# Kernel tuning notes

Hardware: AMD Instinct MI355X
Metric: run time of the kernel (lower is better)

The kernel has to match this reference:

```python
import jax, jax.numpy as jnp
import numpy as np

B, T, I, H = 512, 256, 256, 512

def setup_inputs() -> dict:
    key = jax.random.key(0)
    k1, k2, k3, k4, k5 = jax.random.split(key, 5)
    s = 1.0 / np.sqrt(H + I)
    return {
        "x": jax.random.normal(k1, (B, T, I), dtype=jnp.float32),
        "W_w": jax.random.normal(k2, (4 * H, H + I), dtype=jnp.float32) * s,
        "W_b": jax.random.normal(k3, (4 * H,), dtype=jnp.float32) * s,
        "fc_w": jax.random.normal(k4, (1, H), dtype=jnp.float32) * (1.0 / np.sqrt(H)),
        "fc_b": jax.random.normal(k5, (1,), dtype=jnp.float32) * 0.02,
    }

def reference(x, W_w, W_b, fc_w, fc_b):
    # combined = cat(h_prev, x_t): first H columns of W_w act on h, last I on x
    Wh = W_w[:, :H]          # [4H, H]
    Wx = W_w[:, H:]          # [4H, I]
    # precompute input contributions for all timesteps: [B, T, 4H]
    xW = jnp.einsum('bti,gi->btg', x, Wx) + W_b

    def step(carry, xw_t):
        h, c = carry
        gates = xw_t + h @ Wh.T                      # [B, 4H]
        f, i, o, c_hat = jnp.split(gates, 4, axis=1)  # chunk order f,i,o,c_hat
        f = jax.nn.sigmoid(f)
        i = jax.nn.sigmoid(i)
        o = jax.nn.sigmoid(o)
        c_hat = jnp.tanh(c_hat)
        c_new = f * c + i * c_hat
        h_new = o * jnp.tanh(c_new)
        return (h_new, c_new), None

    h0 = jnp.zeros((x.shape[0], H), dtype=x.dtype)
    c0 = jnp.zeros((x.shape[0], H), dtype=x.dtype)
    (h_T, _), _ = jax.lax.scan(step, (h0, c0), jnp.swapaxes(xW, 0, 1))
    return h_T @ fc_w.T + fc_b                       # [B, 1]
```

## Files before the change

kernel.cpp:

```cpp
#include <hip/hip_runtime.h>
#include <hip/hip_bf16.h>
#include <stdint.h>


#define B_SZ 512
#define T_SZ 256
#define I_SZ 256
#define H_SZ 512
#define K_SZ 768
#define BH   (B_SZ * H_SZ)

typedef float  f32x4  __attribute__((ext_vector_type(4)));
typedef __bf16 bf16x8 __attribute__((ext_vector_type(8)));

__device__ __forceinline__ float fast_sigmoid(float v) {
  return __builtin_amdgcn_rcpf(1.0f + __expf(-v));
}
__device__ __forceinline__ float fast_tanh(float v) {
  return 1.0f - 2.0f * __builtin_amdgcn_rcpf(1.0f + __expf(2.0f * v));
}

#define HLOAD(dst, off) \
  asm volatile("global_load_dwordx4 %0, %1, off offset:" off " sc0 sc1" \
               : "=v"(dst) : "v"(hsrc) : "memory")
#define HSTORE(off, val) \
  asm volatile("global_store_short %0, %1, off offset:" off " sc0 sc1" \
               :: "v"(hdst), "v"(val) : "memory")

__global__ __launch_bounds__(256, 1)
void lstm_persist(const float* __restrict__ x,
                  const float* __restrict__ Ww,
                  const float* __restrict__ Wb,
                  __bf16* __restrict__ hbuf,
                  float* __restrict__ hf32,
                  unsigned int* __restrict__ flags)
{
  __shared__ bf16x8 bw[96 * 64];

  const int wg    = blockIdx.x;
  const int chunk = wg & 7;
  const int jb    = wg >> 3;
  const int tid   = threadIdx.x;
  const int wv    = tid >> 6;
  const int ln    = tid & 63;
  const int l16   = ln & 15;
  const int lhi   = ln >> 4;

  const int colW = jb * 16 + l16;

  for (int c = wv; c < 96; c += 4) {
    const int kt = c >> 2;
    const int nt = c & 3;
    const int k0 = kt * 32 + lhi * 8;
    const float* wr = Ww + (size_t)(nt * 512 + colW) * K_SZ + k0;
    const float4 w0 = *(const float4*)(wr);
    const float4 w1 = *(const float4*)(wr + 4);
    bf16x8 v;
    v[0]=(__bf16)w0.x; v[1]=(__bf16)w0.y; v[2]=(__bf16)w0.z; v[3]=(__bf16)w0.w;
    v[4]=(__bf16)w1.x; v[5]=(__bf16)w1.y; v[6]=(__bf16)w1.z; v[7]=(__bf16)w1.w;
    bw[c * 64 + ln] = v;
  }

  const float bias0 = Wb[0 * 512 + colW];
  const float bias1 = Wb[1 * 512 + colW];
  const float bias2 = Wb[2 * 512 + colW];
  const float bias3 = Wb[3 * 512 + colW];

  __syncthreads();

  const int rowA = chunk * 64 + wv * 16 + l16;
  const int rowD = chunk * 64 + wv * 16 + lhi * 4;
  const float* xlane = x + (size_t)rowA * T_SZ * I_SZ + lhi * 8;
  unsigned int* fbase = flags + (chunk * 4 + wv) * 32;
  const unsigned int* fspin = fbase + (ln & 31);
  unsigned int* fq = fbase + jb;
  __bf16* hb0 = hbuf;
  __bf16* hb1 = hbuf + BH;

  float cst[4] = {0.f, 0.f, 0.f, 0.f};

  auto xpart = [&](f32x4 (&accN)[4], int tn) {
#pragma unroll
    for (int nt = 0; nt < 4; ++nt) accN[nt] = (f32x4){0.f, 0.f, 0.f, 0.f};
    const float* xr = xlane + (size_t)tn * I_SZ;
#pragma unroll
    for (int q = 0; q < 8; ++q) {
      const float4 a0 = *(const float4*)(xr + q * 32);
      const float4 a1 = *(const float4*)(xr + q * 32 + 4);
      bf16x8 a;
      a[0]=(__bf16)a0.x; a[1]=(__bf16)a0.y; a[2]=(__bf16)a0.z; a[3]=(__bf16)a0.w;
      a[4]=(__bf16)a1.x; a[5]=(__bf16)a1.y; a[6]=(__bf16)a1.z; a[7]=(__bf16)a1.w;
#pragma unroll
      for (int nt = 0; nt < 4; ++nt)
        accN[nt] = __builtin_amdgcn_mfma_f32_16x16x32_bf16(
                     a, bw[((16 + q) * 4 + nt) * 64 + ln], accN[nt], 0, 0, 0);
    }
  };

  auto step = [&](f32x4 (&acc)[4], f32x4 (&accN)[4], int t) {
    if (t > 0) {
      unsigned fv;
      do {
        asm volatile("global_load_dword %0, %1, off sc0 sc1\n\t"
                     "s_waitcnt vmcnt(0)"
                     : "=v"(fv) : "v"(fspin) : "memory");
      } while (__any((int)(fv < (unsigned)t)));

      const __bf16* hsrc = ((t & 1) ? hb1 : hb0)
                           + (size_t)rowA * H_SZ + lhi * 8;
      bf16x8 hf[16];
      HLOAD(hf[0],  "0");   HLOAD(hf[1],  "64");  HLOAD(hf[2],  "128");
      HLOAD(hf[3],  "192"); HLOAD(hf[4],  "256"); HLOAD(hf[5],  "320");
      HLOAD(hf[6],  "384"); HLOAD(hf[7],  "448"); HLOAD(hf[8],  "512");
      HLOAD(hf[9],  "576"); HLOAD(hf[10], "640"); HLOAD(hf[11], "704");
      HLOAD(hf[12], "768"); HLOAD(hf[13], "832"); HLOAD(hf[14], "896");
      HLOAD(hf[15], "960");
      asm volatile("s_waitcnt vmcnt(0)" ::: "memory");
      __builtin_amdgcn_sched_barrier(0);
#pragma unroll
      for (int kt = 0; kt < 16; ++kt) {
#pragma unroll
        for (int nt = 0; nt < 4; ++nt)
          acc[nt] = __builtin_amdgcn_mfma_f32_16x16x32_bf16(
                      hf[kt], bw[(kt * 4 + nt) * 64 + ln], acc[nt], 0, 0, 0);
      }
    }

    float hnv[4];
#pragma unroll
    for (int r = 0; r < 4; ++r) {
      const float fg = fast_sigmoid(acc[0][r] + bias0);
      const float ig = fast_sigmoid(acc[1][r] + bias1);
      const float og = fast_sigmoid(acc[2][r] + bias2);
      const float gg = fast_tanh(acc[3][r] + bias3);
      const float cn = fg * cst[r] + ig * gg;
      cst[r] = cn;
      hnv[r] = og * fast_tanh(cn);
    }

    if (t < T_SZ - 1) {
      __bf16* hdst = ((t & 1) ? hb0 : hb1) + (size_t)rowD * H_SZ + colW;
      const unsigned u0 = __builtin_bit_cast(unsigned short, (__bf16)hnv[0]);
      const unsigned u1 = __builtin_bit_cast(unsigned short, (__bf16)hnv[1]);
      const unsigned u2 = __builtin_bit_cast(unsigned short, (__bf16)hnv[2]);
      const unsigned u3 = __builtin_bit_cast(unsigned short, (__bf16)hnv[3]);
      HSTORE("0",    u0);
      HSTORE("1024", u1);
      HSTORE("2048", u2);
      HSTORE("3072", u3);
      asm volatile("s_waitcnt vmcnt(0)" ::: "memory");
      if (ln == 0) {
        const unsigned tv = (unsigned)(t + 1);
        asm volatile("global_store_dword %0, %1, off sc0 sc1"
                     :: "v"(fq), "v"(tv) : "memory");
      }
      xpart(accN, t + 1);
    } else {
#pragma unroll
      for (int r = 0; r < 4; ++r)
        hf32[(size_t)(rowD + r) * H_SZ + colW] = hnv[r];
    }
  };

  f32x4 accA[4], accB[4];
  xpart(accA, 0);
  for (int t2 = 0; t2 < T_SZ; t2 += 2) {
    step(accA, accB, t2);
    step(accB, accA, t2 + 1);
  }
}

__global__ __launch_bounds__(256)
void fc_head(const float* __restrict__ hf32, const float* __restrict__ fcw,
             const float* __restrict__ fcb, float* __restrict__ out)
{
  const int b = blockIdx.x * 256 + threadIdx.x;
  if (b >= B_SZ) return;
  const float4* hp = (const float4*)(hf32 + (size_t)b * H_SZ);
  const float4* wp = (const float4*)fcw;
  float s = 0.f;
#pragma unroll 8
  for (int j = 0; j < H_SZ / 4; ++j) {
    const float4 h = hp[j];
    const float4 w = wp[j];
    s += h.x * w.x + h.y * w.y + h.z * w.z + h.w * w.w;
  }
  out[b] = s + fcb[0];
}

extern "C" void kernel_launch(void* const* d_in, const int* in_sizes, int n_in,
                              void* d_out, int out_size, void* d_ws, size_t ws_size,
                              hipStream_t stream) {
  const float* x   = (const float*)d_in[0];
  const float* Ww  = (const float*)d_in[1];
  const float* Wb  = (const float*)d_in[2];
  const float* fcw = (const float*)d_in[3];
  const float* fcb = (const float*)d_in[4];
  float* out = (float*)d_out;

  char* ws = (char*)d_ws;
  unsigned int* flags = (unsigned int*)ws;
  __bf16* hbuf = (__bf16*)(ws + 4096);
  float*  hf32 = (float*)(ws + 4096 + (size_t)2 * BH * sizeof(__bf16));

  hipMemsetAsync(ws, 0, 4096, stream);

  lstm_persist<<<256, 256, 0, stream>>>(x, Ww, Wb, hbuf, hf32, flags);
  fc_head<<<2, 256, 0, stream>>>(hf32, fcw, fcb, out);
}
```

Measured before the change: 2.107 ms.

## Use per-timestep hidden-state history buffer with cached loads and prefetch x

When the workspace is large enough, each timestep writes h to its own slice of a buffer holding all timesteps, instead of ping-ponging between two buffers. Since every address is written once, the h reads can be plain vector loads rather than inline-asm loads that bypass the cache (sc0 sc1). Separately, the x row for the step after next is loaded into registers ahead of time, so its global-load latency overlaps the recurrence instead of sitting on the critical path. The costs are about 133 MB of extra workspace, more register pressure from the prefetch buffers, and reliance on no stale cache lines existing for addresses that were never read before.

```diff
diff --git a/kernel.cpp b/kernel.cpp
--- a/kernel.cpp
+++ b/kernel.cpp
@@ -27,11 +27,12 @@
   asm volatile("global_store_short %0, %1, off offset:" off " sc0 sc1" \
                :: "v"(hdst), "v"(val) : "memory")
 
+template <bool FAST>
 __global__ __launch_bounds__(256, 1)
 void lstm_persist(const float* __restrict__ x,
                   const float* __restrict__ Ww,
                   const float* __restrict__ Wb,
-                  __bf16* __restrict__ hbuf,
+                  __bf16* __restrict__ hbase,
                   float* __restrict__ hf32,
                   unsigned int* __restrict__ flags)
 {
@@ -74,22 +75,30 @@
   unsigned int* fbase = flags + (chunk * 4 + wv) * 32;
   const unsigned int* fspin = fbase + (ln & 31);
   unsigned int* fq = fbase + jb;
-  __bf16* hb0 = hbuf;
-  __bf16* hb1 = hbuf + BH;
 
   float cst[4] = {0.f, 0.f, 0.f, 0.f};
 
-  auto xpart = [&](f32x4 (&accN)[4], int tn) {
+  float4 xp0[8], xp1[8];
+  auto xprefetch = [&](int tn) {
+    if (tn >= T_SZ) return;
+    const float* xr = xlane + (size_t)tn * I_SZ;
+#pragma unroll
+    for (int q = 0; q < 8; ++q) {
+      xp0[q] = *(const float4*)(xr + q * 32);
+      xp1[q] = *(const float4*)(xr + q * 32 + 4);
+    }
+  };
+
+  auto xpart = [&](f32x4 (&accN)[4]) {
 #pragma unroll
     for (int nt = 0; nt < 4; ++nt) accN[nt] = (f32x4){0.f, 0.f, 0.f, 0.f};
-    const float* xr = xlane + (size_t)tn * I_SZ;
 #pragma unroll
     for (int q = 0; q < 8; ++q) {
-      const float4 a0 = *(const float4*)(xr + q * 32);
-      const float4 a1 = *(const float4*)(xr + q * 32 + 4);
       bf16x8 a;
-      a[0]=(__bf16)a0.x; a[1]=(__bf16)a0.y; a[2]=(__bf16)a0.z; a[3]=(__bf16)a0.w;
-      a[4]=(__bf16)a1.x; a[5]=(__bf16)a1.y; a[6]=(__bf16)a1.z; a[7]=(__bf16)a1.w;
+      a[0]=(__bf16)xp0[q].x; a[1]=(__bf16)xp0[q].y;
+      a[2]=(__bf16)xp0[q].z; a[3]=(__bf16)xp0[q].w;
+      a[4]=(__bf16)xp1[q].x; a[5]=(__bf16)xp1[q].y;
+      a[6]=(__bf16)xp1[q].z; a[7]=(__bf16)xp1[q].w;
 #pragma unroll
       for (int nt = 0; nt < 4; ++nt)
         accN[nt] = __builtin_amdgcn_mfma_f32_16x16x32_bf16(
@@ -106,17 +115,24 @@
                      : "=v"(fv) : "v"(fspin) : "memory");
       } while (__any((int)(fv < (unsigned)t)));
 
-      const __bf16* hsrc = ((t & 1) ? hb1 : hb0)
-                           + (size_t)rowA * H_SZ + lhi * 8;
       bf16x8 hf[16];
-      HLOAD(hf[0],  "0");   HLOAD(hf[1],  "64");  HLOAD(hf[2],  "128");
-      HLOAD(hf[3],  "192"); HLOAD(hf[4],  "256"); HLOAD(hf[5],  "320");
-      HLOAD(hf[6],  "384"); HLOAD(hf[7],  "448"); HLOAD(hf[8],  "512");
-      HLOAD(hf[9],  "576"); HLOAD(hf[10], "640"); HLOAD(hf[11], "704");
-      HLOAD(hf[12], "768"); HLOAD(hf[13], "832"); HLOAD(hf[14], "896");
-      HLOAD(hf[15], "960");
-      asm volatile("s_waitcnt vmcnt(0)" ::: "memory");
-      __builtin_amdgcn_sched_barrier(0);
+      if constexpr (FAST) {
+        const bf16x8* hrow = (const bf16x8*)(hbase + (size_t)(t - 1) * BH
+                                             + (size_t)rowA * H_SZ) + lhi;
+#pragma unroll
+        for (int kt = 0; kt < 16; ++kt) hf[kt] = hrow[kt * 4];
+      } else {
+        const __bf16* hsrc = hbase + (size_t)(t & 1) * BH
+                                   + (size_t)rowA * H_SZ + lhi * 8;
+        HLOAD(hf[0],  "0");   HLOAD(hf[1],  "64");  HLOAD(hf[2],  "128");
+        HLOAD(hf[3],  "192"); HLOAD(hf[4],  "256"); HLOAD(hf[5],  "320");
+        HLOAD(hf[6],  "384"); HLOAD(hf[7],  "448"); HLOAD(hf[8],  "512");
+        HLOAD(hf[9],  "576"); HLOAD(hf[10], "640"); HLOAD(hf[11], "704");
+        HLOAD(hf[12], "768"); HLOAD(hf[13], "832"); HLOAD(hf[14], "896");
+        HLOAD(hf[15], "960");
+        asm volatile("s_waitcnt vmcnt(0)" ::: "memory");
+        __builtin_amdgcn_sched_barrier(0);
+      }
 #pragma unroll
       for (int kt = 0; kt < 16; ++kt) {
 #pragma unroll
@@ -139,7 +155,9 @@
     }
 
     if (t < T_SZ - 1) {
-      __bf16* hdst = ((t & 1) ? hb0 : hb1) + (size_t)rowD * H_SZ + colW;
+      __bf16* hdst = (FAST ? hbase + (size_t)t * BH
+                           : hbase + (size_t)((t + 1) & 1) * BH)
+                     + (size_t)rowD * H_SZ + colW;
       const unsigned u0 = __builtin_bit_cast(unsigned short, (__bf16)hnv[0]);
       const unsigned u1 = __builtin_bit_cast(unsigned short, (__bf16)hnv[1]);
       const unsigned u2 = __builtin_bit_cast(unsigned short, (__bf16)hnv[2]);
@@ -154,7 +172,8 @@
         asm volatile("global_store_dword %0, %1, off sc0 sc1"
                      :: "v"(fq), "v"(tv) : "memory");
       }
-      xpart(accN, t + 1);
+      xpart(accN);
+      xprefetch(t + 2);
     } else {
 #pragma unroll
       for (int r = 0; r < 4; ++r)
@@ -163,7 +182,9 @@
   };
 
   f32x4 accA[4], accB[4];
-  xpart(accA, 0);
+  xprefetch(0);
+  xpart(accA);
+  xprefetch(1);
   for (int t2 = 0; t2 < T_SZ; t2 += 2) {
     step(accA, accB, t2);
     step(accB, accA, t2 + 1);
@@ -200,11 +221,22 @@
 
   char* ws = (char*)d_ws;
   unsigned int* flags = (unsigned int*)ws;
-  __bf16* hbuf = (__bf16*)(ws + 4096);
-  float*  hf32 = (float*)(ws + 4096 + (size_t)2 * BH * sizeof(__bf16));
+
+  const size_t hbytes = (size_t)(T_SZ - 1) * BH * sizeof(__bf16);
+  const size_t need   = 4096 + hbytes + (size_t)BH * sizeof(float);
+  const bool fast = (ws_size >= need);
 
   hipMemsetAsync(ws, 0, 4096, stream);
 
-  lstm_persist<<<256, 256, 0, stream>>>(x, Ww, Wb, hbuf, hf32, flags);
-  fc_head<<<2, 256, 0, stream>>>(hf32, fcw, fcb, out);
-}
+  if (fast) {
+    __bf16* hbase = (__bf16*)(ws + 4096);
+    float*  hf32  = (float*)(ws + 4096 + hbytes);
+    lstm_persist<true><<<256, 256, 0, stream>>>(x, Ww, Wb, hbase, hf32, flags);
+    fc_head<<<2, 256, 0, stream>>>(hf32, fcw, fcb, out);
+  } else {
+    __bf16* hbase = (__bf16*)(ws + 4096);
+    float*  hf32  = (float*)(ws + 4096 + (size_t)2 * BH * sizeof(__bf16));
+    lstm_persist<false><<<256, 256, 0, stream>>>(x, Ww, Wb, hbase, hf32, flags);
+    fc_head<<<2, 256, 0, stream>>>(hf32, fcw, fcb, out);
+  }
+}
```

Measured after the change: 1.781 ms. -15.5%, faster.
